# Kernel optimization log

Hardware: AMD Instinct MI355X
Metric: run time of the kernel (lower is better)

The kernel has to match this reference:

```python
import jax, jax.numpy as jnp
import numpy as np

NUM_EXPERTS = 8
HIDDEN = 2048
INTER = 1408
TOKENS = 2048
TOP_K = 2


def setup_inputs() -> dict:
    key = jax.random.key(0)
    ks = jax.random.split(key, 6)
    s_h = 1.0 / np.sqrt(HIDDEN)
    s_i = 1.0 / np.sqrt(INTER)
    hidden_states = jax.random.normal(ks[0], (TOKENS, HIDDEN), dtype=jnp.float32)
    top_k_index = jax.random.randint(ks[1], (TOKENS, TOP_K), 0, NUM_EXPERTS)
    w = jax.random.uniform(ks[2], (TOKENS, TOP_K), dtype=jnp.float32)
    top_k_weights = w / jnp.sum(w, axis=-1, keepdims=True)
    # weights stored as [E, in, out] for einsum (torch Linear is [out, in])
    gate_w = jax.random.uniform(ks[3], (NUM_EXPERTS, HIDDEN, INTER), jnp.float32, -s_h, s_h)
    up_w = jax.random.uniform(ks[4], (NUM_EXPERTS, HIDDEN, INTER), jnp.float32, -s_h, s_h)
    down_w = jax.random.uniform(ks[5], (NUM_EXPERTS, INTER, HIDDEN), jnp.float32, -s_i, s_i)
    return {
        "hidden_states": hidden_states,
        "top_k_index": top_k_index,
        "top_k_weights": top_k_weights,
        "gate_w": gate_w,
        "up_w": up_w,
        "down_w": down_w,
    }


def reference(hidden_states, top_k_index, top_k_weights, gate_w, up_w, down_w):
    # combine weight per (expert, token): w_et = sum_k topk_w[t,k] * [idx[t,k]==e]
    one_hot = jax.nn.one_hot(top_k_index, NUM_EXPERTS, dtype=hidden_states.dtype)  # [T,K,E]
    combine = jnp.einsum("tk,tke->et", top_k_weights, one_hot)  # [E,T]
    # dense per-expert SwiGLU MLP over all tokens (mask-combine form of the
    # gather/scatter loop; identical math since combine weight is 0 for
    # non-routed (expert, token) pairs)
    g = jnp.einsum("th,ehi->eti", hidden_states, gate_w)  # [E,T,I]
    u = jnp.einsum("th,ehi->eti", hidden_states, up_w)
    y = jnp.einsum("eti,eih->eth", jax.nn.silu(g) * u, down_w)  # [E,T,H]
    out = jnp.einsum("et,eth->th", combine, y)  # [T,H]
    return out
```

## Files before the change

kernel.cpp:

```cpp
#include <hip/hip_runtime.h>
#include <cstdint>
#include <cstddef>

#define NE 8
#define HD 2048
#define IN 1408
#define NT 2048
#define NP (NT*2)
#define MAXMT 40

typedef __bf16 bf16;
typedef __bf16 bf16x8 __attribute__((ext_vector_type(8)));
typedef __bf16 bf16x4 __attribute__((ext_vector_type(4)));
typedef float f32x4 __attribute__((ext_vector_type(4)));

__device__ __forceinline__ void load_lds16(const void* g, void* l) {
  __builtin_amdgcn_global_load_lds((const __attribute__((address_space(1))) uint32_t*)g,
                                   (__attribute__((address_space(3))) uint32_t*)l, 16, 0, 0);
}

__global__ void k_cvt(const float* __restrict__ x, bf16* __restrict__ y) {
  int i = blockIdx.x * 256 + threadIdx.x;
  f32x4 v = ((const f32x4*)x)[i];
  bf16x4 o;
  o[0] = (bf16)v[0]; o[1] = (bf16)v[1]; o[2] = (bf16)v[2]; o[3] = (bf16)v[3];
  ((bf16x4*)y)[i] = o;
}

__global__ void k_route(const int* __restrict__ idx, const float* __restrict__ w,
                        int* __restrict__ perm_tok, float* __restrict__ perm_w,
                        int* __restrict__ slot_of, int* __restrict__ tiles) {
  __shared__ int cnt[NE], off[NE + 1], rk[NE];
  int tid = threadIdx.x;
  if (tid < NE) { cnt[tid] = 0; rk[tid] = 0; }
  __syncthreads();
  for (int a = tid; a < NP; a += 256) atomicAdd(&cnt[idx[a]], 1);
  __syncthreads();
  if (tid == 0) { off[0] = 0; for (int e = 0; e < NE; e++) off[e + 1] = off[e] + cnt[e]; }
  __syncthreads();
  for (int a = tid; a < NP; a += 256) {
    int e = idx[a];
    int p = off[e] + atomicAdd(&rk[e], 1);
    perm_tok[p] = a >> 1;
    perm_w[p] = w[a];
    slot_of[a] = p;
  }
  __syncthreads();
  if (tid == 0) {
    int n = 0;
    for (int e = 0; e < NE; e++)
      for (int r = off[e]; r < off[e + 1]; r += 128) {
        tiles[n] = e; tiles[MAXMT + n] = r; tiles[2 * MAXMT + n] = off[e + 1];
        n++;
      }
    for (int s = n; s < MAXMT; s++) tiles[s] = -1;
  }
}

__launch_bounds__(256, 2)
__global__ void k_gemm1(const bf16* __restrict__ hid, const float* __restrict__ gw,
                        const float* __restrict__ uw, const int* __restrict__ perm_tok,
                        const float* __restrict__ perm_w, const int* __restrict__ tiles,
                        bf16* __restrict__ act) {
  int b = blockIdx.x;
  int q = b >> 5, r5 = b & 31;
  int p = q * 8 + (r5 & 7);
  if (p >= 110) return;
  int slot = (p / 11) * 4 + (r5 >> 3);
  int e = tiles[slot];
  if (e < 0) return;
  int nt = p % 11;
  int row0 = tiles[MAXMT + slot], rowend = tiles[2 * MAXMT + slot];
  int nb = nt * 128;

  __shared__ bf16 As[128 * 64];
  __shared__ bf16 Bg[128 * 64];
  __shared__ bf16 Bu[128 * 64];

  int tid = threadIdx.x;
  int lane = tid & 63, wave = tid >> 6;
  int wm = (wave >> 1) * 64, wn = (wave & 1) * 64;

  const bf16* aG[4]; bf16* aL[4];
#pragma unroll
  for (int i2 = 0; i2 < 4; i2++) {
    int s = i2 * 256 + tid;
    int r = s >> 3, c = (s & 7) ^ (r & 7);
    int tr = row0 + r; if (tr > NP - 1) tr = NP - 1;
    aG[i2] = hid + (size_t)perm_tok[tr] * HD + c * 8;
    aL[i2] = As + s * 8;
  }
  int kk = (tid & 7) * 8, nn = (tid >> 3) * 4;
  const float* gB = gw + (size_t)e * HD * IN + (size_t)kk * IN + (nb + nn);
  const float* uB = uw + (size_t)e * HD * IN + (size_t)kk * IN + (nb + nn);
  int bslot[4];
#pragma unroll
  for (int i2 = 0; i2 < 4; i2++) { int n = nn + i2; bslot[i2] = (n * 8 + ((tid & 7) ^ (n & 7))) * 8; }

  f32x4 accG[4][4] = {};
  f32x4 accU[4][4] = {};

  for (int k0 = 0; k0 < HD; k0 += 64) {
    __syncthreads();
#pragma unroll
    for (int i2 = 0; i2 < 4; i2++) load_lds16(aG[i2] + k0, aL[i2]);
    {
      f32x4 v[8];
#pragma unroll
      for (int j = 0; j < 8; j++) v[j] = *(const f32x4*)(gB + (size_t)(k0 + j) * IN);
#pragma unroll
      for (int i2 = 0; i2 < 4; i2++) {
        bf16x8 o;
#pragma unroll
        for (int j = 0; j < 8; j++) o[j] = (bf16)v[j][i2];
        *(bf16x8*)(Bg + bslot[i2]) = o;
      }
#pragma unroll
      for (int j = 0; j < 8; j++) v[j] = *(const f32x4*)(uB + (size_t)(k0 + j) * IN);
#pragma unroll
      for (int i2 = 0; i2 < 4; i2++) {
        bf16x8 o;
#pragma unroll
        for (int j = 0; j < 8; j++) o[j] = (bf16)v[j][i2];
        *(bf16x8*)(Bu + bslot[i2]) = o;
      }
    }
    __syncthreads();
#pragma unroll
    for (int ks = 0; ks < 2; ks++) {
      int ckf = ks * 4 + (lane >> 4);
      bf16x8 af[4], bgf[4], buf[4];
#pragma unroll
      for (int fm = 0; fm < 4; fm++) {
        int m = wm + fm * 16 + (lane & 15);
        af[fm] = *(const bf16x8*)(As + (m * 8 + (ckf ^ (m & 7))) * 8);
      }
#pragma unroll
      for (int fn = 0; fn < 4; fn++) {
        int n = wn + fn * 16 + (lane & 15);
        int sl = (n * 8 + (ckf ^ (n & 7))) * 8;
        bgf[fn] = *(const bf16x8*)(Bg + sl);
        buf[fn] = *(const bf16x8*)(Bu + sl);
      }
#pragma unroll
      for (int fm = 0; fm < 4; fm++)
#pragma unroll
        for (int fn = 0; fn < 4; fn++) {
          accG[fm][fn] = __builtin_amdgcn_mfma_f32_16x16x32_bf16(af[fm], bgf[fn], accG[fm][fn], 0, 0, 0);
          accU[fm][fn] = __builtin_amdgcn_mfma_f32_16x16x32_bf16(af[fm], buf[fn], accU[fm][fn], 0, 0, 0);
        }
    }
  }
#pragma unroll
  for (int fm = 0; fm < 4; fm++) {
#pragma unroll
    for (int rr = 0; rr < 4; rr++) {
      int m = wm + fm * 16 + ((lane >> 4) << 2) + rr;
      int row = row0 + m;
      if (row < rowend) {
        float pw = perm_w[row];
#pragma unroll
        for (int fn = 0; fn < 4; fn++) {
          int n = nb + wn + fn * 16 + (lane & 15);
          float g = accG[fm][fn][rr], u = accU[fm][fn][rr];
          float sv = g / (1.0f + __expf(-g));
          act[(size_t)row * IN + n] = (bf16)(sv * u * pw);
        }
      }
    }
  }
}

__launch_bounds__(256, 2)
__global__ void k_gemm2(const bf16* __restrict__ act, const float* __restrict__ dw,
                        const int* __restrict__ tiles, float* __restrict__ pout) {
  int b = blockIdx.x;
  int q = b >> 5, r5 = b & 31;
  int p = q * 8 + (r5 & 7);
  int slot = (p >> 4) * 4 + (r5 >> 3);
  int e = tiles[slot];
  if (e < 0) return;
  int nt = p & 15;
  int row0 = tiles[MAXMT + slot], rowend = tiles[2 * MAXMT + slot];
  int nb = nt * 128;

  __shared__ bf16 As[128 * 64];
  __shared__ bf16 Bd[128 * 64];

  int tid = threadIdx.x;
  int lane = tid & 63, wave = tid >> 6;
  int wm = (wave >> 1) * 64, wn = (wave & 1) * 64;

  const bf16* aG[4]; bf16* aL[4];
#pragma unroll
  for (int i2 = 0; i2 < 4; i2++) {
    int s = i2 * 256 + tid;
    int r = s >> 3, c = (s & 7) ^ (r & 7);
    int ar = row0 + r; if (ar > NP - 1) ar = NP - 1;
    aG[i2] = act + (size_t)ar * IN + c * 8;
    aL[i2] = As + s * 8;
  }
  int kk = (tid & 7) * 8, nn = (tid >> 3) * 4;
  const float* dB = dw + (size_t)e * IN * HD + (size_t)kk * HD + (nb + nn);
  int bslot[4];
#pragma unroll
  for (int i2 = 0; i2 < 4; i2++) { int n = nn + i2; bslot[i2] = (n * 8 + ((tid & 7) ^ (n & 7))) * 8; }

  f32x4 acc[4][4] = {};

  for (int k0 = 0; k0 < IN; k0 += 64) {
    __syncthreads();
#pragma unroll
    for (int i2 = 0; i2 < 4; i2++) load_lds16(aG[i2] + k0, aL[i2]);
    {
      f32x4 v[8];
#pragma unroll
      for (int j = 0; j < 8; j++) v[j] = *(const f32x4*)(dB + (size_t)(k0 + j) * HD);
#pragma unroll
      for (int i2 = 0; i2 < 4; i2++) {
        bf16x8 o;
#pragma unroll
        for (int j = 0; j < 8; j++) o[j] = (bf16)v[j][i2];
        *(bf16x8*)(Bd + bslot[i2]) = o;
      }
    }
    __syncthreads();
#pragma unroll
    for (int ks = 0; ks < 2; ks++) {
      int ckf = ks * 4 + (lane >> 4);
      bf16x8 af[4], bdf[4];
#pragma unroll
      for (int fm = 0; fm < 4; fm++) {
        int m = wm + fm * 16 + (lane & 15);
        af[fm] = *(const bf16x8*)(As + (m * 8 + (ckf ^ (m & 7))) * 8);
      }
#pragma unroll
      for (int fn = 0; fn < 4; fn++) {
        int n = wn + fn * 16 + (lane & 15);
        bdf[fn] = *(const bf16x8*)(Bd + (n * 8 + (ckf ^ (n & 7))) * 8);
      }
#pragma unroll
      for (int fm = 0; fm < 4; fm++)
#pragma unroll
        for (int fn = 0; fn < 4; fn++)
          acc[fm][fn] = __builtin_amdgcn_mfma_f32_16x16x32_bf16(af[fm], bdf[fn], acc[fm][fn], 0, 0, 0);
    }
  }
#pragma unroll
  for (int fm = 0; fm < 4; fm++) {
#pragma unroll
    for (int rr = 0; rr < 4; rr++) {
      int m = wm + fm * 16 + ((lane >> 4) << 2) + rr;
      int row = row0 + m;
      if (row < rowend) {
#pragma unroll
        for (int fn = 0; fn < 4; fn++) {
          int n = nb + wn + fn * 16 + (lane & 15);
          pout[(size_t)row * HD + n] = acc[fm][fn][rr];
        }
      }
    }
  }
}

__global__ void k_comb(const float* __restrict__ pout, const int* __restrict__ slot_of,
                       float* __restrict__ out) {
  int i = blockIdx.x * 256 + threadIdx.x;
  int t = i >> 9;
  int hc = i & 511;
  f32x4 a = ((const f32x4*)(pout + (size_t)slot_of[2 * t] * HD))[hc];
  f32x4 c = ((const f32x4*)(pout + (size_t)slot_of[2 * t + 1] * HD))[hc];
  ((f32x4*)(out + (size_t)t * HD))[hc] = a + c;
}

extern "C" void kernel_launch(void* const* d_in, const int* in_sizes, int n_in,
                              void* d_out, int out_size, void* d_ws, size_t ws_size,
                              hipStream_t stream) {
  const float* hidden  = (const float*)d_in[0];
  const int*   tk_idx  = (const int*)d_in[1];
  const float* tk_w    = (const float*)d_in[2];
  const float* gw      = (const float*)d_in[3];
  const float* uw      = (const float*)d_in[4];
  const float* dw      = (const float*)d_in[5];
  float* out = (float*)d_out;

  char* ws = (char*)d_ws;
  int*   perm_tok = (int*)ws;
  float* perm_w   = (float*)(ws + 16384);
  int*   slot_of  = (int*)(ws + 32768);
  int*   tiles    = (int*)(ws + 49152);
  bf16*  hid_bf   = (bf16*)(ws + 53248);
  bf16*  act      = (bf16*)(ws + 53248 + 8388608);
  float* pout     = (float*)(ws + 53248 + 8388608 + 11534336);

  k_cvt  <<<4096, 256, 0, stream>>>(hidden, hid_bf);
  k_route<<<1,    256, 0, stream>>>(tk_idx, tk_w, perm_tok, perm_w, slot_of, tiles);
  k_gemm1<<<448,  256, 0, stream>>>(hid_bf, gw, uw, perm_tok, perm_w, tiles, act);
  k_gemm2<<<640,  256, 0, stream>>>(act, dw, tiles, pout);
  k_comb <<<4096, 256, 0, stream>>>(pout, slot_of, out);
}
```

Baseline: 479.6 us.

## Double-buffer GEMM pipeline and split gate/up into separate GEMM launches

Replaces the two GEMM kernels with a shared double-buffered template that prefetches the next K-slab's A (LDS direct load) and B (fp32 registers) while MFMAs run on the current buffer. It also sets MFMA priority. The fused gate+up GEMM is split into two independent blocks per tile, each writing fp32 g/u to workspace, with a new elementwise kernel applying SiLU*up*weight to produce bf16 activations. This doubles the block count for GEMM1 and hides load latency, at the cost of extra fp32 round-trip traffic for g/u, re-reading the gathered A tile twice, and an additional launch.

Result: slower. 496.8 us (+3.6%).

```diff
diff --git a/kernel.cpp b/kernel.cpp
--- a/kernel.cpp
+++ b/kernel.cpp
@@ -19,6 +19,12 @@
                                    (__attribute__((address_space(3))) uint32_t*)l, 16, 0, 0);
 }
 
+#define PIPE_BAR() do { \
+    asm volatile("s_waitcnt vmcnt(0) lgkmcnt(0)" ::: "memory"); \
+    __builtin_amdgcn_s_barrier(); \
+    __builtin_amdgcn_sched_barrier(0); \
+  } while (0)
+
 __global__ void k_cvt(const float* __restrict__ x, bf16* __restrict__ y) {
   int i = blockIdx.x * 256 + threadIdx.x;
   f32x4 v = ((const f32x4*)x)[i];
@@ -57,100 +63,97 @@
   }
 }
 
-__launch_bounds__(256, 2)
-__global__ void k_gemm1(const bf16* __restrict__ hid, const float* __restrict__ gw,
-                        const float* __restrict__ uw, const int* __restrict__ perm_tok,
-                        const float* __restrict__ perm_w, const int* __restrict__ tiles,
-                        bf16* __restrict__ act) {
-  int b = blockIdx.x;
-  int q = b >> 5, r5 = b & 31;
-  int p = q * 8 + (r5 & 7);
-  if (p >= 110) return;
-  int slot = (p / 11) * 4 + (r5 >> 3);
-  int e = tiles[slot];
-  if (e < 0) return;
-  int nt = p % 11;
-  int row0 = tiles[MAXMT + slot], rowend = tiles[2 * MAXMT + slot];
-  int nb = nt * 128;
-
-  __shared__ bf16 As[128 * 64];
-  __shared__ bf16 Bg[128 * 64];
-  __shared__ bf16 Bu[128 * 64];
+template<int KTOT, int NTOT, bool GATHER>
+__device__ __forceinline__ void mm_pipe(const bf16* __restrict__ A,
+                                        const float* __restrict__ Bsrc,
+                                        const int* __restrict__ perm_tok,
+                                        int row0, int rowend, int nb,
+                                        float* __restrict__ C) {
+  __shared__ __align__(16) bf16 As[2][128 * 64];
+  __shared__ __align__(16) bf16 Bs[2][128 * 64];
 
   int tid = threadIdx.x;
   int lane = tid & 63, wave = tid >> 6;
   int wm = (wave >> 1) * 64, wn = (wave & 1) * 64;
 
-  const bf16* aG[4]; bf16* aL[4];
+  const bf16* aG[4]; int aOff[4];
 #pragma unroll
   for (int i2 = 0; i2 < 4; i2++) {
     int s = i2 * 256 + tid;
     int r = s >> 3, c = (s & 7) ^ (r & 7);
     int tr = row0 + r; if (tr > NP - 1) tr = NP - 1;
-    aG[i2] = hid + (size_t)perm_tok[tr] * HD + c * 8;
-    aL[i2] = As + s * 8;
+    int arow = GATHER ? perm_tok[tr] : tr;
+    aG[i2] = A + (size_t)arow * KTOT + c * 8;
+    aOff[i2] = s * 8;
   }
   int kk = (tid & 7) * 8, nn = (tid >> 3) * 4;
-  const float* gB = gw + (size_t)e * HD * IN + (size_t)kk * IN + (nb + nn);
-  const float* uB = uw + (size_t)e * HD * IN + (size_t)kk * IN + (nb + nn);
+  const float* gB = Bsrc + (size_t)kk * NTOT + (nb + nn);
   int bslot[4];
 #pragma unroll
   for (int i2 = 0; i2 < 4; i2++) { int n = nn + i2; bslot[i2] = (n * 8 + ((tid & 7) ^ (n & 7))) * 8; }
 
-  f32x4 accG[4][4] = {};
-  f32x4 accU[4][4] = {};
-
-  for (int k0 = 0; k0 < HD; k0 += 64) {
-    __syncthreads();
-#pragma unroll
-    for (int i2 = 0; i2 < 4; i2++) load_lds16(aG[i2] + k0, aL[i2]);
-    {
-      f32x4 v[8];
-#pragma unroll
-      for (int j = 0; j < 8; j++) v[j] = *(const f32x4*)(gB + (size_t)(k0 + j) * IN);
+  f32x4 acc[4][4] = {};
+  f32x4 v[8];
+
+#pragma unroll
+  for (int i2 = 0; i2 < 4; i2++) load_lds16(aG[i2], &As[0][aOff[i2]]);
+#pragma unroll
+  for (int j = 0; j < 8; j++) v[j] = *(const f32x4*)(gB + (size_t)j * NTOT);
+#pragma unroll
+  for (int i2 = 0; i2 < 4; i2++) {
+    bf16x8 o;
+#pragma unroll
+    for (int j = 0; j < 8; j++) o[j] = (bf16)v[j][i2];
+    *(bf16x8*)(&Bs[0][bslot[i2]]) = o;
+  }
+  PIPE_BAR();
+
+  const int NK = KTOT / 64;
+  int cur = 0;
+#pragma unroll 2
+  for (int k = 0; k < NK; k++) {
+    if (k + 1 < NK) {
+      int k0n = (k + 1) * 64;
+#pragma unroll
+      for (int j = 0; j < 8; j++) v[j] = *(const f32x4*)(gB + (size_t)(k0n + j) * NTOT);
+#pragma unroll
+      for (int i2 = 0; i2 < 4; i2++) load_lds16(aG[i2] + k0n, &As[cur ^ 1][aOff[i2]]);
+    }
+#pragma unroll
+    for (int ks = 0; ks < 2; ks++) {
+      int ckf = ks * 4 + (lane >> 4);
+      bf16x8 af[4], bfr[4];
+#pragma unroll
+      for (int fm = 0; fm < 4; fm++) {
+        int m = wm + fm * 16 + (lane & 15);
+        af[fm] = *(const bf16x8*)(&As[cur][(m * 8 + (ckf ^ (m & 7))) * 8]);
+      }
+#pragma unroll
+      for (int fn = 0; fn < 4; fn++) {
+        int n = wn + fn * 16 + (lane & 15);
+        bfr[fn] = *(const bf16x8*)(&Bs[cur][(n * 8 + (ckf ^ (n & 7))) * 8]);
+      }
+      __builtin_amdgcn_s_setprio(1);
+#pragma unroll
+      for (int fm = 0; fm < 4; fm++)
+#pragma unroll
+        for (int fn = 0; fn < 4; fn++)
+          acc[fm][fn] = __builtin_amdgcn_mfma_f32_16x16x32_bf16(af[fm], bfr[fn], acc[fm][fn], 0, 0, 0);
+      __builtin_amdgcn_s_setprio(0);
+    }
+    if (k + 1 < NK) {
 #pragma unroll
       for (int i2 = 0; i2 < 4; i2++) {
         bf16x8 o;
 #pragma unroll
         for (int j = 0; j < 8; j++) o[j] = (bf16)v[j][i2];
-        *(bf16x8*)(Bg + bslot[i2]) = o;
-      }
-#pragma unroll
-      for (int j = 0; j < 8; j++) v[j] = *(const f32x4*)(uB + (size_t)(k0 + j) * IN);
-#pragma unroll
-      for (int i2 = 0; i2 < 4; i2++) {
-        bf16x8 o;
-#pragma unroll
-        for (int j = 0; j < 8; j++) o[j] = (bf16)v[j][i2];
-        *(bf16x8*)(Bu + bslot[i2]) = o;
-      }
-    }
-    __syncthreads();
-#pragma unroll
-    for (int ks = 0; ks < 2; ks++) {
-      int ckf = ks * 4 + (lane >> 4);
-      bf16x8 af[4], bgf[4], buf[4];
-#pragma unroll
-      for (int fm = 0; fm < 4; fm++) {
-        int m = wm + fm * 16 + (lane & 15);
-        af[fm] = *(const bf16x8*)(As + (m * 8 + (ckf ^ (m & 7))) * 8);
-      }
-#pragma unroll
-      for (int fn = 0; fn < 4; fn++) {
-        int n = wn + fn * 16 + (lane & 15);
-        int sl = (n * 8 + (ckf ^ (n & 7))) * 8;
-        bgf[fn] = *(const bf16x8*)(Bg + sl);
-        buf[fn] = *(const bf16x8*)(Bu + sl);
-      }
-#pragma unroll
-      for (int fm = 0; fm < 4; fm++)
-#pragma unroll
-        for (int fn = 0; fn < 4; fn++) {
-          accG[fm][fn] = __builtin_amdgcn_mfma_f32_16x16x32_bf16(af[fm], bgf[fn], accG[fm][fn], 0, 0, 0);
-          accU[fm][fn] = __builtin_amdgcn_mfma_f32_16x16x32_bf16(af[fm], buf[fn], accU[fm][fn], 0, 0, 0);
-        }
-    }
-  }
+        *(bf16x8*)(&Bs[cur ^ 1][bslot[i2]]) = o;
+      }
+    }
+    PIPE_BAR();
+    cur ^= 1;
+  }
+
 #pragma unroll
   for (int fm = 0; fm < 4; fm++) {
 #pragma unroll
@@ -158,13 +161,10 @@
       int m = wm + fm * 16 + ((lane >> 4) << 2) + rr;
       int row = row0 + m;
       if (row < rowend) {
-        float pw = perm_w[row];
 #pragma unroll
         for (int fn = 0; fn < 4; fn++) {
           int n = nb + wn + fn * 16 + (lane & 15);
-          float g = accG[fm][fn][rr], u = accU[fm][fn][rr];
-          float sv = g / (1.0f + __expf(-g));
-          act[(size_t)row * IN + n] = (bf16)(sv * u * pw);
+          C[(size_t)row * NTOT + n] = acc[fm][fn][rr];
         }
       }
     }
@@ -172,95 +172,52 @@
 }
 
 __launch_bounds__(256, 2)
-__global__ void k_gemm2(const bf16* __restrict__ act, const float* __restrict__ dw,
-                        const int* __restrict__ tiles, float* __restrict__ pout) {
+__global__ void k_mm1(const bf16* __restrict__ hid, const float* __restrict__ gw,
+                      const float* __restrict__ uw, const int* __restrict__ perm_tok,
+                      const int* __restrict__ tiles,
+                      float* __restrict__ g, float* __restrict__ u) {
   int b = blockIdx.x;
-  int q = b >> 5, r5 = b & 31;
-  int p = q * 8 + (r5 & 7);
-  int slot = (p >> 4) * 4 + (r5 >> 3);
+  int half = b >= 440 ? 1 : 0;
+  int b2 = b - half * 440;
+  int slot = b2 / 11, nt = b2 % 11;
   int e = tiles[slot];
   if (e < 0) return;
-  int nt = p & 15;
   int row0 = tiles[MAXMT + slot], rowend = tiles[2 * MAXMT + slot];
-  int nb = nt * 128;
-
-  __shared__ bf16 As[128 * 64];
-  __shared__ bf16 Bd[128 * 64];
-
-  int tid = threadIdx.x;
-  int lane = tid & 63, wave = tid >> 6;
-  int wm = (wave >> 1) * 64, wn = (wave & 1) * 64;
-
-  const bf16* aG[4]; bf16* aL[4];
-#pragma unroll
-  for (int i2 = 0; i2 < 4; i2++) {
-    int s = i2 * 256 + tid;
-    int r = s >> 3, c = (s & 7) ^ (r & 7);
-    int ar = row0 + r; if (ar > NP - 1) ar = NP - 1;
-    aG[i2] = act + (size_t)ar * IN + c * 8;
-    aL[i2] = As + s * 8;
-  }
-  int kk = (tid & 7) * 8, nn = (tid >> 3) * 4;
-  const float* dB = dw + (size_t)e * IN * HD + (size_t)kk * HD + (nb + nn);
-  int bslot[4];
-#pragma unroll
-  for (int i2 = 0; i2 < 4; i2++) { int n = nn + i2; bslot[i2] = (n * 8 + ((tid & 7) ^ (n & 7))) * 8; }
-
-  f32x4 acc[4][4] = {};
-
-  for (int k0 = 0; k0 < IN; k0 += 64) {
-    __syncthreads();
-#pragma unroll
-    for (int i2 = 0; i2 < 4; i2++) load_lds16(aG[i2] + k0, aL[i2]);
-    {
-      f32x4 v[8];
-#pragma unroll
-      for (int j = 0; j < 8; j++) v[j] = *(const f32x4*)(dB + (size_t)(k0 + j) * HD);
-#pragma unroll
-      for (int i2 = 0; i2 < 4; i2++) {
-        bf16x8 o;
-#pragma unroll
-        for (int j = 0; j < 8; j++) o[j] = (bf16)v[j][i2];
-        *(bf16x8*)(Bd + bslot[i2]) = o;
-      }
-    }
-    __syncthreads();
-#pragma unroll
-    for (int ks = 0; ks < 2; ks++) {
-      int ckf = ks * 4 + (lane >> 4);
-      bf16x8 af[4], bdf[4];
-#pragma unroll
-      for (int fm = 0; fm < 4; fm++) {
-        int m = wm + fm * 16 + (lane & 15);
-        af[fm] = *(const bf16x8*)(As + (m * 8 + (ckf ^ (m & 7))) * 8);
-      }
-#pragma unroll
-      for (int fn = 0; fn < 4; fn++) {
-        int n = wn + fn * 16 + (lane & 15);
-        bdf[fn] = *(const bf16x8*)(Bd + (n * 8 + (ckf ^ (n & 7))) * 8);
-      }
-#pragma unroll
-      for (int fm = 0; fm < 4; fm++)
-#pragma unroll
-        for (int fn = 0; fn < 4; fn++)
-          acc[fm][fn] = __builtin_amdgcn_mfma_f32_16x16x32_bf16(af[fm], bdf[fn], acc[fm][fn], 0, 0, 0);
-    }
-  }
-#pragma unroll
-  for (int fm = 0; fm < 4; fm++) {
-#pragma unroll
-    for (int rr = 0; rr < 4; rr++) {
-      int m = wm + fm * 16 + ((lane >> 4) << 2) + rr;
-      int row = row0 + m;
-      if (row < rowend) {
-#pragma unroll
-        for (int fn = 0; fn < 4; fn++) {
-          int n = nb + wn + fn * 16 + (lane & 15);
-          pout[(size_t)row * HD + n] = acc[fm][fn][rr];
-        }
-      }
-    }
-  }
+  const float* B = (half ? uw : gw) + (size_t)e * HD * IN;
+  float* C = half ? u : g;
+  mm_pipe<HD, IN, true>(hid, B, perm_tok, row0, rowend, nt * 128, C);
+}
+
+__global__ void k_act(const float* __restrict__ g, const float* __restrict__ u,
+                      const float* __restrict__ pw, bf16* __restrict__ act) {
+  int i = blockIdx.x * 256 + threadIdx.x;
+  int row = i / (IN / 8);
+  float w = pw[row];
+  f32x4 g0 = ((const f32x4*)g)[2 * i], g1 = ((const f32x4*)g)[2 * i + 1];
+  f32x4 u0 = ((const f32x4*)u)[2 * i], u1 = ((const f32x4*)u)[2 * i + 1];
+  bf16x8 o;
+#pragma unroll
+  for (int j = 0; j < 4; j++) {
+    float s = g0[j] / (1.0f + __expf(-g0[j]));
+    o[j] = (bf16)(s * u0[j] * w);
+  }
+#pragma unroll
+  for (int j = 0; j < 4; j++) {
+    float s = g1[j] / (1.0f + __expf(-g1[j]));
+    o[4 + j] = (bf16)(s * u1[j] * w);
+  }
+  ((bf16x8*)act)[i] = o;
+}
+
+__launch_bounds__(256, 2)
+__global__ void k_mm2(const bf16* __restrict__ act, const float* __restrict__ dw,
+                      const int* __restrict__ tiles, float* __restrict__ pout) {
+  int b = blockIdx.x;
+  int slot = b >> 4, nt = b & 15;
+  int e = tiles[slot];
+  if (e < 0) return;
+  int row0 = tiles[MAXMT + slot], rowend = tiles[2 * MAXMT + slot];
+  mm_pipe<IN, HD, false>(act, dw + (size_t)e * IN * HD, nullptr, row0, rowend, nt * 128, pout);
 }
 
 __global__ void k_comb(const float* __restrict__ pout, const int* __restrict__ slot_of,
@@ -291,11 +248,15 @@
   int*   tiles    = (int*)(ws + 49152);
   bf16*  hid_bf   = (bf16*)(ws + 53248);
   bf16*  act      = (bf16*)(ws + 53248 + 8388608);
-  float* pout     = (float*)(ws + 53248 + 8388608 + 11534336);
+  char*  xbase    = ws + 53248 + 8388608 + 11534336;
+  float* gbuf     = (float*)xbase;
+  float* ubuf     = (float*)(xbase + 23068672);
+  float* pout     = (float*)xbase;
 
   k_cvt  <<<4096, 256, 0, stream>>>(hidden, hid_bf);
   k_route<<<1,    256, 0, stream>>>(tk_idx, tk_w, perm_tok, perm_w, slot_of, tiles);
-  k_gemm1<<<448,  256, 0, stream>>>(hid_bf, gw, uw, perm_tok, perm_w, tiles, act);
-  k_gemm2<<<640,  256, 0, stream>>>(act, dw, tiles, pout);
+  k_mm1  <<<880,  256, 0, stream>>>(hid_bf, gw, uw, perm_tok, tiles, gbuf, ubuf);
+  k_act  <<<2816, 256, 0, stream>>>(gbuf, ubuf, perm_w, act);
+  k_mm2  <<<640,  256, 0, stream>>>(act, dw, tiles, pout);
   k_comb <<<4096, 256, 0, stream>>>(pout, slot_of, out);
 }
```
